# Optimization experiments

Measured on AMD Instinct MI355X. Metric: run time of the kernel, lower is better.

Reference implementation:

```python
import jax, jax.numpy as jnp
import numpy as np

B, T, I, H, O = 256, 1024, 64, 256, 8

def setup_inputs() -> dict:
    key = jax.random.key(0)
    ks = jax.random.split(key, 11)
    s_in = 1.0 / np.sqrt(I + H)
    s_h = 1.0 / np.sqrt(H)
    return {
        "x": jax.random.normal(ks[0], (B, T, I), dtype=jnp.float32),
        "W_f": jax.random.uniform(ks[1], (I + H, H), jnp.float32, -s_in, s_in),
        "b_f": jax.random.uniform(ks[2], (H,), jnp.float32, -s_in, s_in),
        "W_i": jax.random.uniform(ks[3], (I + H, H), jnp.float32, -s_in, s_in),
        "b_i": jax.random.uniform(ks[4], (H,), jnp.float32, -s_in, s_in),
        "W_c": jax.random.uniform(ks[5], (I + H, H), jnp.float32, -s_in, s_in),
        "b_c": jax.random.uniform(ks[6], (H,), jnp.float32, -s_in, s_in),
        "W_o": jax.random.uniform(ks[7], (I + H, H), jnp.float32, -s_in, s_in),
        "b_o": jax.random.uniform(ks[8], (H,), jnp.float32, -s_in, s_in),
        "W_ho": jax.random.uniform(ks[9], (H, O), jnp.float32, -s_h, s_h),
        "b_ho": jax.random.uniform(ks[10], (O,), jnp.float32, -s_h, s_h),
    }

def reference(x, W_f, b_f, W_i, b_i, W_c, b_c, W_o, b_o, W_ho, b_ho):
    # Fuse the 4 gate linears into one GEMM per step: combined @ [W_f|W_i|W_c|W_o]
    Wg = jnp.concatenate([W_f, W_i, W_c, W_o], axis=1)   # [I+H, 4H]
    bg = jnp.concatenate([b_f, b_i, b_c, b_o], axis=0)   # [4H]
    Hd = W_f.shape[1]
    h0 = jnp.zeros((x.shape[0], Hd), dtype=x.dtype)
    c0 = jnp.zeros((x.shape[0], Hd), dtype=x.dtype)

    def step(carry, x_t):
        h, c = carry
        combined = jnp.concatenate([h, x_t], axis=1)      # [B, H+I], h first (as in torch code)
        g = combined @ Wg + bg                            # [B, 4H]
        f = jax.nn.sigmoid(g[:, 0*Hd:1*Hd])
        i = jax.nn.sigmoid(g[:, 1*Hd:2*Hd])
        c_hat = jnp.tanh(g[:, 2*Hd:3*Hd])
        o = jax.nn.sigmoid(g[:, 3*Hd:4*Hd])
        c_new = f * c + i * c_hat
        h_new = o * jnp.tanh(c_new)
        return (h_new, c_new), None

    (h_T, _), _ = jax.lax.scan(step, (h0, c0), jnp.swapaxes(x, 0, 1))
    return h_T @ W_ho + b_ho
```

## Files before the change

### kernel.cpp

```cpp
#include <hip/hip_runtime.h>
#include <math.h>

constexpr int Bsz = 256, Tsz = 1024, Isz = 64, Hsz = 256, Osz = 8;
constexpr int NB  = 4;
constexpr int K   = Hsz + Isz;

__global__ __launch_bounds__(256) void lstm_fused(
    const float* __restrict__ x,
    const float* __restrict__ W_f, const float* __restrict__ b_f,
    const float* __restrict__ W_i, const float* __restrict__ b_i,
    const float* __restrict__ W_c, const float* __restrict__ b_c,
    const float* __restrict__ W_o, const float* __restrict__ b_o,
    const float* __restrict__ W_ho, const float* __restrict__ b_ho,
    float* __restrict__ out)
{
    __shared__ float comb[NB][K];
    const int j  = threadIdx.x;
    const int b0 = blockIdx.x * NB;

    #pragma unroll
    for (int b = 0; b < NB; ++b) comb[b][j] = 0.0f;
    {
        const int b = j >> 6, i = j & 63;
        comb[b][Hsz + i] = x[((size_t)(b0 + b) * Tsz) * Isz + i];
    }
    __syncthreads();

    float c[NB];
    #pragma unroll
    for (int b = 0; b < NB; ++b) c[b] = 0.0f;

    const float bf = b_f[j], bi = b_i[j], bc = b_c[j], bo = b_o[j];

    for (int t = 0; t < Tsz; ++t) {
        float gf[NB], gi[NB], gc[NB], go[NB];
        #pragma unroll
        for (int b = 0; b < NB; ++b) { gf[b] = bf; gi[b] = bi; gc[b] = bc; go[b] = bo; }

        #pragma unroll 4
        for (int k = 0; k < K; ++k) {
            const float wf = W_f[k * Hsz + j];
            const float wi = W_i[k * Hsz + j];
            const float wc = W_c[k * Hsz + j];
            const float wo = W_o[k * Hsz + j];
            #pragma unroll
            for (int b = 0; b < NB; ++b) {
                const float v = comb[b][k];
                gf[b] = fmaf(v, wf, gf[b]);
                gi[b] = fmaf(v, wi, gi[b]);
                gc[b] = fmaf(v, wc, gc[b]);
                go[b] = fmaf(v, wo, go[b]);
            }
        }
        __syncthreads();

        #pragma unroll
        for (int b = 0; b < NB; ++b) {
            const float f  = 1.0f / (1.0f + expf(-gf[b]));
            const float ig = 1.0f / (1.0f + expf(-gi[b]));
            const float ch = tanhf(gc[b]);
            const float og = 1.0f / (1.0f + expf(-go[b]));
            c[b] = f * c[b] + ig * ch;
            comb[b][j] = og * tanhf(c[b]);
        }
        if (t + 1 < Tsz) {
            const int b = j >> 6, i2 = j & 63;
            comb[b][Hsz + i2] = x[((size_t)(b0 + b) * Tsz + (t + 1)) * Isz + i2];
        }
        __syncthreads();
    }

    if (j < NB * Osz) {
        const int b = j >> 3, o = j & 7;
        float acc = b_ho[o];
        #pragma unroll 8
        for (int k = 0; k < Hsz; ++k)
            acc = fmaf(comb[b][k], W_ho[k * Osz + o], acc);
        out[(size_t)(b0 + b) * Osz + o] = acc;
    }
}

extern "C" void kernel_launch(void* const* d_in, const int* in_sizes, int n_in,
                              void* d_out, int out_size, void* d_ws, size_t ws_size,
                              hipStream_t stream) {
    const float* x    = (const float*)d_in[0];
    const float* W_f  = (const float*)d_in[1];
    const float* b_f  = (const float*)d_in[2];
    const float* W_i  = (const float*)d_in[3];
    const float* b_i  = (const float*)d_in[4];
    const float* W_c  = (const float*)d_in[5];
    const float* b_c  = (const float*)d_in[6];
    const float* W_o  = (const float*)d_in[7];
    const float* b_o  = (const float*)d_in[8];
    const float* W_ho = (const float*)d_in[9];
    const float* b_ho = (const float*)d_in[10];
    float* out = (float*)d_out;

    lstm_fused<<<Bsz / NB, 256, 0, stream>>>(
        x, W_f, b_f, W_i, b_i, W_c, b_c, W_o, b_o, W_ho, b_ho, out);
}
```

Baseline: 22.98 ms.

## Split hidden dimension across 4 cooperating blocks with register-resident weights and global sync

Each batch group of 4 sequences is now handled by 4 blocks, and each block owns 64 hidden columns. Each thread keeps its 320 weights for one gate in registers instead of reloading them from global memory every step. Blocks exchange their h slices each step through a double-buffered global buffer and an atomic counter with spin-waiting. The own-slice and x contributions are computed before waiting, so part of the matmul overlaps the sync. This quadruples the number of blocks and removes the repeated weight traffic. In exchange it adds inter-block synchronization latency and depends on all 256 blocks being co-resident, with a spin cap that could silently proceed on stale data.

```diff
diff --git a/kernel.cpp b/kernel.cpp
--- a/kernel.cpp
+++ b/kernel.cpp
@@ -2,100 +2,207 @@
 #include <math.h>
 
 constexpr int Bsz = 256, Tsz = 1024, Isz = 64, Hsz = 256, Osz = 8;
-constexpr int NB  = 4;
-constexpr int K   = Hsz + Isz;
-
-__global__ __launch_bounds__(256) void lstm_fused(
+constexpr int NB = 4;
+constexpr int NG = 4;
+constexpr int K  = Hsz + Isz;
+constexpr int SPIN_CAP = 1 << 14;
+
+#define SCOPE_AGENT __HIP_MEMORY_SCOPE_AGENT
+
+#define FMA4(vv, warr, base)                      \
+  acc[b] = fmaf(vv.x, warr[(base)+0], acc[b]);    \
+  acc[b] = fmaf(vv.y, warr[(base)+1], acc[b]);    \
+  acc[b] = fmaf(vv.z, warr[(base)+2], acc[b]);    \
+  acc[b] = fmaf(vv.w, warr[(base)+3], acc[b]);
+
+__global__ __launch_bounds__(256, 1) void lstm_ws_kernel(
     const float* __restrict__ x,
     const float* __restrict__ W_f, const float* __restrict__ b_f,
     const float* __restrict__ W_i, const float* __restrict__ b_i,
     const float* __restrict__ W_c, const float* __restrict__ b_c,
     const float* __restrict__ W_o, const float* __restrict__ b_o,
     const float* __restrict__ W_ho, const float* __restrict__ b_ho,
-    float* __restrict__ out)
+    float* __restrict__ out, int* __restrict__ cnt, float* __restrict__ Hbuf)
 {
     __shared__ float comb[NB][K];
+    __shared__ float gat[4][NB][64];
+
     const int j  = threadIdx.x;
-    const int b0 = blockIdx.x * NB;
+    const int g  = blockIdx.x >> 6;
+    const int bg = blockIdx.x & 63;
+    const int b0 = bg * NB;
+    const int q  = j >> 6;
+    const int m  = j & 63;
+    const int hcol = g * 64 + m;
+
+    const float* Wq  = (q == 0) ? W_f : (q == 1) ? W_i : (q == 2) ? W_c : W_o;
+    const float* bqp = (q == 0) ? b_f : (q == 1) ? b_i : (q == 2) ? b_c : b_o;
+    const float bias = bqp[hcol];
+
+    float wOwn[64], wOth[192], wX[64];
+    #pragma unroll
+    for (int kk = 0; kk < 64; ++kk) wOwn[kk] = Wq[(g * 64 + kk) * Hsz + hcol];
+    #pragma unroll
+    for (int r = 1; r < 4; ++r) {
+        const int kb = ((g + r) & 3) * 64;
+        #pragma unroll
+        for (int kk = 0; kk < 64; ++kk)
+            wOth[(r - 1) * 64 + kk] = Wq[(kb + kk) * Hsz + hcol];
+    }
+    #pragma unroll
+    for (int kk = 0; kk < 64; ++kk) wX[kk] = Wq[(Hsz + kk) * Hsz + hcol];
 
     #pragma unroll
     for (int b = 0; b < NB; ++b) comb[b][j] = 0.0f;
-    {
-        const int b = j >> 6, i = j & 63;
-        comb[b][Hsz + i] = x[((size_t)(b0 + b) * Tsz) * Isz + i];
-    }
+    comb[j >> 6][Hsz + m] = x[((size_t)(b0 + (j >> 6)) * Tsz + 0) * Isz + m];
+    float cstate = 0.0f;
     __syncthreads();
 
-    float c[NB];
-    #pragma unroll
-    for (int b = 0; b < NB; ++b) c[b] = 0.0f;
-
-    const float bf = b_f[j], bi = b_i[j], bc = b_c[j], bo = b_o[j];
+    int* mycnt = cnt + bg;
 
     for (int t = 0; t < Tsz; ++t) {
-        float gf[NB], gi[NB], gc[NB], go[NB];
-        #pragma unroll
-        for (int b = 0; b < NB; ++b) { gf[b] = bf; gi[b] = bi; gc[b] = bc; go[b] = bo; }
-
-        #pragma unroll 4
-        for (int k = 0; k < K; ++k) {
-            const float wf = W_f[k * Hsz + j];
-            const float wi = W_i[k * Hsz + j];
-            const float wc = W_c[k * Hsz + j];
-            const float wo = W_o[k * Hsz + j];
+        float acc[NB];
+        #pragma unroll
+        for (int b = 0; b < NB; ++b) acc[b] = bias;
+
+        const int ob = g * 64;
+        #pragma unroll
+        for (int c4 = 0; c4 < 16; ++c4) {
             #pragma unroll
             for (int b = 0; b < NB; ++b) {
-                const float v = comb[b][k];
-                gf[b] = fmaf(v, wf, gf[b]);
-                gi[b] = fmaf(v, wi, gi[b]);
-                gc[b] = fmaf(v, wc, gc[b]);
-                go[b] = fmaf(v, wo, go[b]);
-            }
-        }
-        __syncthreads();
-
-        #pragma unroll
-        for (int b = 0; b < NB; ++b) {
-            const float f  = 1.0f / (1.0f + expf(-gf[b]));
-            const float ig = 1.0f / (1.0f + expf(-gi[b]));
-            const float ch = tanhf(gc[b]);
-            const float og = 1.0f / (1.0f + expf(-go[b]));
-            c[b] = f * c[b] + ig * ch;
-            comb[b][j] = og * tanhf(c[b]);
-        }
-        if (t + 1 < Tsz) {
-            const int b = j >> 6, i2 = j & 63;
-            comb[b][Hsz + i2] = x[((size_t)(b0 + b) * Tsz + (t + 1)) * Isz + i2];
-        }
-        __syncthreads();
+                const float4 v = *(const float4*)&comb[b][ob + c4 * 4];
+                FMA4(v, wOwn, c4 * 4)
+            }
+        }
+        #pragma unroll
+        for (int c4 = 0; c4 < 16; ++c4) {
+            #pragma unroll
+            for (int b = 0; b < NB; ++b) {
+                const float4 v = *(const float4*)&comb[b][Hsz + c4 * 4];
+                FMA4(v, wX, c4 * 4)
+            }
+        }
+
+        if (t) {
+            if (j == 0) {
+                int it = 0;
+                while (__hip_atomic_load(mycnt, __ATOMIC_ACQUIRE, SCOPE_AGENT) < 4 * t
+                       && it++ < SPIN_CAP)
+                    __builtin_amdgcn_s_sleep(8);
+            }
+            __syncthreads();
+            {
+                const int b = j >> 6;
+                if ((m >> 4) != g) {
+                    const float* src = Hbuf + ((((size_t)((t - 1) & 1)) * 64 + bg) * 4 + b) * 256;
+                    const int col = 4 * m;
+                    const float a0 = __hip_atomic_load(src + col + 0, __ATOMIC_RELAXED, SCOPE_AGENT);
+                    const float a1 = __hip_atomic_load(src + col + 1, __ATOMIC_RELAXED, SCOPE_AGENT);
+                    const float a2 = __hip_atomic_load(src + col + 2, __ATOMIC_RELAXED, SCOPE_AGENT);
+                    const float a3 = __hip_atomic_load(src + col + 3, __ATOMIC_RELAXED, SCOPE_AGENT);
+                    comb[b][col + 0] = a0; comb[b][col + 1] = a1;
+                    comb[b][col + 2] = a2; comb[b][col + 3] = a3;
+                }
+            }
+            __syncthreads();
+        }
+
+        #pragma unroll
+        for (int r = 0; r < 3; ++r) {
+            const int kb = ((g + r + 1) & 3) * 64;
+            #pragma unroll
+            for (int c4 = 0; c4 < 16; ++c4) {
+                #pragma unroll
+                for (int b = 0; b < NB; ++b) {
+                    const float4 v = *(const float4*)&comb[b][kb + c4 * 4];
+                    FMA4(v, wOth, r * 64 + c4 * 4)
+                }
+            }
+        }
+
+        float xv;
+        {
+            const int tt = (t + 1 < Tsz) ? t + 1 : t;
+            xv = x[((size_t)(b0 + (j >> 6)) * Tsz + tt) * Isz + m];
+        }
+
+        #pragma unroll
+        for (int b = 0; b < NB; ++b) gat[q][b][m] = acc[b];
+        __syncthreads();
+        {
+            const int b = j >> 6;
+            const float gf = gat[0][b][m], gi = gat[1][b][m];
+            const float gc = gat[2][b][m], go = gat[3][b][m];
+            const float f  = 1.0f / (1.0f + expf(-gf));
+            const float ii = 1.0f / (1.0f + expf(-gi));
+            const float ch = tanhf(gc);
+            const float oo = 1.0f / (1.0f + expf(-go));
+            cstate = f * cstate + ii * ch;
+            const float h = oo * tanhf(cstate);
+            comb[b][g * 64 + m] = h;
+            float* dst = Hbuf + ((((size_t)(t & 1)) * 64 + bg) * 4 + b) * 256 + g * 64 + m;
+            __hip_atomic_store(dst, h, __ATOMIC_RELAXED, SCOPE_AGENT);
+        }
+        comb[j >> 6][Hsz + m] = xv;
+        __syncthreads();
+        if (j == 0)
+            __hip_atomic_fetch_add(mycnt, 1, __ATOMIC_RELEASE, SCOPE_AGENT);
     }
 
-    if (j < NB * Osz) {
-        const int b = j >> 3, o = j & 7;
-        float acc = b_ho[o];
-        #pragma unroll 8
-        for (int k = 0; k < Hsz; ++k)
-            acc = fmaf(comb[b][k], W_ho[k * Osz + o], acc);
-        out[(size_t)(b0 + b) * Osz + o] = acc;
+    if (g == 0) {
+        if (j == 0) {
+            int it = 0;
+            while (__hip_atomic_load(mycnt, __ATOMIC_ACQUIRE, SCOPE_AGENT) < 4 * Tsz
+                   && it++ < SPIN_CAP)
+                __builtin_amdgcn_s_sleep(8);
+        }
+        __syncthreads();
+        {
+            const int b = j >> 6;
+            if ((m >> 4) != 0) {
+                const float* src = Hbuf + ((((size_t)((Tsz - 1) & 1)) * 64 + bg) * 4 + b) * 256;
+                const int col = 4 * m;
+                const float a0 = __hip_atomic_load(src + col + 0, __ATOMIC_RELAXED, SCOPE_AGENT);
+                const float a1 = __hip_atomic_load(src + col + 1, __ATOMIC_RELAXED, SCOPE_AGENT);
+                const float a2 = __hip_atomic_load(src + col + 2, __ATOMIC_RELAXED, SCOPE_AGENT);
+                const float a3 = __hip_atomic_load(src + col + 3, __ATOMIC_RELAXED, SCOPE_AGENT);
+                comb[b][col + 0] = a0; comb[b][col + 1] = a1;
+                comb[b][col + 2] = a2; comb[b][col + 3] = a3;
+            }
+        }
+        __syncthreads();
+        if (j < NB * Osz) {
+            const int b = j >> 3, o = j & 7;
+            float s = b_ho[o];
+            #pragma unroll 8
+            for (int k2 = 0; k2 < Hsz; ++k2)
+                s = fmaf(comb[b][k2], W_ho[k2 * Osz + o], s);
+            out[(size_t)(b0 + b) * Osz + o] = s;
+        }
     }
 }
 
 extern "C" void kernel_launch(void* const* d_in, const int* in_sizes, int n_in,
                               void* d_out, int out_size, void* d_ws, size_t ws_size,
                               hipStream_t stream) {
-    const float* x    = (const float*)d_in[0];
-    const float* W_f  = (const float*)d_in[1];
-    const float* b_f  = (const float*)d_in[2];
-    const float* W_i  = (const float*)d_in[3];
-    const float* b_i  = (const float*)d_in[4];
-    const float* W_c  = (const float*)d_in[5];
-    const float* b_c  = (const float*)d_in[6];
-    const float* W_o  = (const float*)d_in[7];
-    const float* b_o  = (const float*)d_in[8];
-    const float* W_ho = (const float*)d_in[9];
-    const float* b_ho = (const float*)d_in[10];
-    float* out = (float*)d_out;
-
-    lstm_fused<<<Bsz / NB, 256, 0, stream>>>(
-        x, W_f, b_f, W_i, b_i, W_c, b_c, W_o, b_o, W_ho, b_ho, out);
+    const float* xp  = (const float*)d_in[0];
+    const float* wf  = (const float*)d_in[1];
+    const float* bf  = (const float*)d_in[2];
+    const float* wi  = (const float*)d_in[3];
+    const float* bi  = (const float*)d_in[4];
+    const float* wc  = (const float*)d_in[5];
+    const float* bc  = (const float*)d_in[6];
+    const float* wo  = (const float*)d_in[7];
+    const float* bo  = (const float*)d_in[8];
+    const float* who = (const float*)d_in[9];
+    const float* bho = (const float*)d_in[10];
+    float* outp = (float*)d_out;
+
+    int*   cntp  = (int*)d_ws;
+    float* hbufp = (float*)((char*)d_ws + 4096);
+
+    hipMemsetAsync(d_ws, 0, 4096, stream);
+
+    lstm_ws_kernel<<<dim3(NG * 64), dim3(256), 0, stream>>>(
+        xp, wf, bf, wi, bi, wc, bc, wo, bo, who, bho, outp, cntp, hbufp);
 }
```

New measurement: 44.46 ms. +93.5%, slower.
